# Kernel optimization log

Hardware: AMD Instinct MI355X
Metric: run time of the kernel (lower is better)

Reference implementation:

```python
import jax, jax.numpy as jnp
import numpy as np

B, NB, L, K, C, H = 4, 256, 64, 65, 512, 8
HD = C // H
SCALE = HD ** -0.5


def setup_inputs() -> dict:
    key = jax.random.key(0)
    k = jax.random.split(key, 6)
    x = jax.random.normal(k[0], (B, NB * L, C), dtype=jnp.float32)
    mask = jax.random.bernoulli(k[1], 0.3, (NB, L, K))
    d = jnp.arange(L)
    mask = mask.at[:, d, d].set(True)      # self edges always on
    mask = mask.at[:, :, L].set(True)      # block-node column always on
    edge_feats = jax.random.normal(k[2], (NB, L, K, 4), dtype=jnp.float32)
    qkv_w = jax.random.normal(k[3], (C, 3 * C), dtype=jnp.float32) * (C ** -0.5)
    qkv_b = jnp.zeros((3 * C,), dtype=jnp.float32)
    proj_w = jax.random.normal(k[4], (C, C), dtype=jnp.float32) * (C ** -0.5)
    proj_b = jnp.zeros((C,), dtype=jnp.float32)
    return {"x": x, "attn_mask": mask, "edge_feats": edge_feats,
            "qkv_w": qkv_w, "qkv_b": qkv_b, "proj_w": proj_w, "proj_b": proj_b}


def reference(x, attn_mask, edge_feats, qkv_w, qkv_b, proj_w, proj_b):
    # x: (B, N, C) with N = NB*L (no padding needed); pool = 1, layout LxL+1
    x_blk = x.reshape(B, NB, L, C)                       # query tokens per leaf block
    block_node = x_blk.mean(axis=2, keepdims=True)       # (B, NB, 1, C)
    kv = jnp.concatenate([x_blk, block_node], axis=2)    # (B, NB, K, C), K = L+1

    qkv_q = x_blk @ qkv_w + qkv_b
    qkv_kv = kv @ qkv_w + qkv_b
    q = qkv_q[..., :C].reshape(B, NB, L, H, HD)
    k = qkv_kv[..., C:2 * C].reshape(B, NB, K, H, HD)
    v = qkv_kv[..., 2 * C:].reshape(B, NB, K, H, HD)

    scores = jnp.einsum('bnqhd,bnkhd->bnqkh', q, k) * SCALE  # (B,NB,L,K,H)

    # physics bias: edge_feats[..., :4] broadcast over batch; special/diagonal overrides
    bp = jnp.broadcast_to(edge_feats[None, ..., :4], (B, NB, L, K, 4))
    bp = bp.at[:, :, :, L, :].set(0.0)
    bp = bp.at[:, :, :, L, 3].set(1.0)                    # block-node key column
    d = jnp.arange(L)
    bp = bp.at[:, :, d, d, :].set(0.0)
    bp = bp.at[:, :, d, d, 3].set(1.0)                    # self edge
    scores = scores + bp[..., 3:4]                        # channel 3 additive bias (all heads)

    mask = attn_mask[None, :, :, :, None]                 # (1,NB,L,K,1)
    scores = jnp.where(mask, scores, jnp.float32(-1e9))
    attn = jax.nn.softmax(scores, axis=3)

    out = jnp.einsum('bnqkh,bnkhd->bnqhd', attn, v).reshape(B, NB * L, C)
    return out @ proj_w + proj_b
```

## Files before the change

kernel.cpp:

```cpp
#include <hip/hip_runtime.h>
#include <hip/hip_bf16.h>
#include <math.h>

typedef unsigned short u16;
typedef __attribute__((ext_vector_type(8))) short s16x8;
typedef __attribute__((ext_vector_type(4))) float f32x4;

#define NB_ 256
#define L_  64
#define KK_ 65
#define C_  512
#define H_  8
#define NEDGE (256*64*65)
#define MTOT  65536

__device__ __forceinline__ float b2f(u16 u){
  union { unsigned int i; float f; } x; x.i = ((unsigned int)u) << 16; return x.f;
}
__device__ __forceinline__ u16 f2b(float f){
  union { float f; unsigned int i; } x; x.f = f;
  return (u16)((x.i + 0x7FFFu + ((x.i >> 16) & 1u)) >> 16);
}

__device__ __forceinline__ void gload_lds16(const u16* g, u16* l){
  __builtin_amdgcn_global_load_lds(
      (const __attribute__((address_space(1))) unsigned int*)g,
      (__attribute__((address_space(3))) unsigned int*)l,
      16, 0, 0);
}

__global__ void detect_dtype_kernel(const u16* __restrict__ x, int* __restrict__ flagdt){
  __shared__ int cnt;
  if (threadIdx.x == 0) cnt = 0;
  __syncthreads();
  u16 v = x[(size_t)threadIdx.x * 2 * 1001];
  int e = (v >> 7) & 0xFF;
  if (e >= 141) atomicAdd(&cnt, 1);
  __syncthreads();
  if (threadIdx.x == 0) *flagdt = (cnt >= 8) ? 1 : 0;
}

__global__ void detect_mask_kernel(const unsigned char* __restrict__ m, int* __restrict__ flag){
  __shared__ int ok1, ok2, ok4;
  if (threadIdx.x == 0){ ok1 = 1; ok2 = 1; ok4 = 1; }
  __syncthreads();
  size_t e = (size_t)threadIdx.x * 65 + 64;
  if (((const unsigned char*)m)[e] == 0)  atomicAnd(&ok1, 0);
  if (((const unsigned short*)m)[e] == 0) atomicAnd(&ok2, 0);
  if (((const unsigned int*)m)[e] == 0u)  atomicAnd(&ok4, 0);
  __syncthreads();
  if (threadIdx.x == 0){
    int f = 4;
    if (ok2) f = 2;
    if (ok1) f = 1;
    *flag = f;
  }
}

__global__ void convert_kernel(const void* __restrict__ src, u16* __restrict__ dst,
                               long n, const int* __restrict__ flagdt){
  long i = ((long)blockIdx.x * 256 + threadIdx.x) * 8;
  if (i >= n) return;
  if (*flagdt){
    const float* s = (const float*)src + i;
    u16 o[8];
    #pragma unroll
    for (int j = 0; j < 8; ++j) o[j] = f2b(s[j]);
    *(s16x8*)(dst + i) = *(const s16x8*)o;
  } else {
    *(s16x8*)(dst + i) = *(const s16x8*)((const u16*)src + i);
  }
}

__global__ void build_bias_kernel(const void* __restrict__ edge,
                                  const unsigned char* __restrict__ mask,
                                  const int* __restrict__ flagdt,
                                  const int* __restrict__ flagm,
                                  u16* __restrict__ dst){
  long i = (long)blockIdx.x * 256 + threadIdx.x;
  if (i >= NEDGE) return;
  int kk = (int)(i % 65);
  long rowi = i / 65;
  int l = (int)(rowi & 63);
  int fm = *flagm;
  bool mt;
  if (fm == 1)      mt = mask[i] != 0;
  else if (fm == 2) mt = ((const unsigned short*)mask)[i] != 0;
  else              mt = ((const unsigned int*)mask)[i]   != 0u;
  float v;
  if (!mt)                      v = -1e9f;
  else if (kk == 64 || kk == l) v = 1.0f;
  else v = (*flagdt) ? ((const float*)edge)[i*4 + 3] : b2f(((const u16*)edge)[i*4 + 3]);
  dst[i] = f2b(v);
}

__global__ void transpose_conv_kernel(const void* __restrict__ in, u16* __restrict__ out,
                                      int R, int Cc, const int* __restrict__ flagdt){
  long i = (long)blockIdx.x * 256 + threadIdx.x;
  if (i < (long)R * Cc){
    int r = (int)(i / Cc), c = (int)(i % Cc);
    u16 v = (*flagdt) ? f2b(((const float*)in)[i]) : ((const u16*)in)[i];
    out[(long)c * R + r] = v;
  }
}

__global__ __launch_bounds__(256) void block_mean_kernel(const u16* __restrict__ x, u16* __restrict__ bm){
  int blk = blockIdx.x;
  const u16* xp = x + (long)blk * 64 * 512;
  for (int c = threadIdx.x; c < 512; c += 256){
    float s = 0.f;
    #pragma unroll
    for (int l = 0; l < 64; ++l) s += b2f(xp[l*512 + c]);
    bm[(long)blk * 512 + c] = f2b(s * 0.015625f);
  }
}

__global__ __launch_bounds__(256) void gemm_bt_kernel(
    const u16* __restrict__ A, const u16* __restrict__ BT,
    const u16* __restrict__ bias, u16* __restrict__ Cmat,
    int lda, int ldc, int Kdim, const int* __restrict__ flagdt, int out_mode,
    long row_off)
{
  __shared__ __align__(16) u16 As[128*32];
  __shared__ __align__(16) u16 Bs[128*32];
  const int t = threadIdx.x;
  const int lane = t & 63;
  const int w = t >> 6;
  const int wm = w & 1, wn = w >> 1;
  const int quad = lane >> 4;
  const int ml = lane & 15;

  const int nwg  = gridDim.x * gridDim.y;
  const int orig = blockIdx.y * gridDim.x + blockIdx.x;
  int lid = orig;
  if ((nwg & 7) == 0) lid = (orig & 7) * (nwg >> 3) + (orig >> 3);
  const int bx = lid % gridDim.x;
  const int by = lid / gridDim.x;
  const long colbase = (long)bx * 128;
  const long rowbase = (long)by * 128;
  const int of = out_mode ? *flagdt : 0;

  const f32x4 zero4 = {0.f, 0.f, 0.f, 0.f};
  f32x4 acc[4][4];
  #pragma unroll
  for (int i = 0; i < 4; ++i)
    #pragma unroll
    for (int j = 0; j < 4; ++j) acc[i][j] = zero4;

  const int c0 = t,       r0 = c0 >> 2, s0 = c0 & 3, g0 = s0 ^ ((r0 >> 1) & 3);
  const int c1 = t + 256, r1 = c1 >> 2, s1 = c1 & 3, g1 = s1 ^ ((r1 >> 1) & 3);
  const u16* Arow0 = A + (rowbase + r0) * (long)lda + g0*8;
  const u16* Arow1 = A + (rowbase + r1) * (long)lda + g1*8;
  const u16* Brow0 = BT + (colbase + r0) * (long)Kdim + g0*8;
  const u16* Brow1 = BT + (colbase + r1) * (long)Kdim + g1*8;

  u16* AsW0 = As + w*512;
  u16* AsW1 = As + 2048 + w*512;
  u16* BsW0 = Bs + w*512;
  u16* BsW1 = Bs + 2048 + w*512;

  for (int k0 = 0; k0 < Kdim; k0 += 32){
    __syncthreads();
    gload_lds16(Arow0 + k0, AsW0);
    gload_lds16(Arow1 + k0, AsW1);
    gload_lds16(Brow0 + k0, BsW0);
    gload_lds16(Brow1 + k0, BsW1);
    __syncthreads();
    s16x8 af[4], bfr[4];
    #pragma unroll
    for (int i = 0; i < 4; ++i){
      int m = wm*64 + i*16 + ml;
      af[i]  = *(const s16x8*)(As + m*32 + ((quad ^ ((m>>1)&3)))*8);
      int n = wn*64 + i*16 + ml;
      bfr[i] = *(const s16x8*)(Bs + n*32 + ((quad ^ ((n>>1)&3)))*8);
    }
    #pragma unroll
    for (int i = 0; i < 4; ++i)
      #pragma unroll
      for (int j = 0; j < 4; ++j)
        acc[i][j] = __builtin_amdgcn_mfma_f32_16x16x32_bf16(af[i], bfr[j], acc[i][j], 0, 0, 0);
  }

  #pragma unroll
  for (int j = 0; j < 4; ++j){
    long col = colbase + wn*64 + j*16 + ml;
    float bv = b2f(bias[col]);
    #pragma unroll
    for (int i = 0; i < 4; ++i){
      long row = row_off + rowbase + wm*64 + i*16 + quad*4;
      if (of){
        float* Cf = (float*)Cmat;
        #pragma unroll
        for (int r = 0; r < 4; ++r)
          Cf[(row + r) * (long)ldc + col] = acc[i][j][r] + bv;
      } else {
        #pragma unroll
        for (int r = 0; r < 4; ++r)
          Cmat[(row + r) * (long)ldc + col] = f2b(acc[i][j][r] + bv);
      }
    }
  }
}

__global__ __launch_bounds__(256, 4) void attn_kernel(
    const u16* __restrict__ Y, const u16* __restrict__ kvb,
    const u16* __restrict__ biasb, u16* __restrict__ AO)
{
  __shared__ __align__(16) u16 k_s [80*72];
  __shared__ __align__(16) u16 vT_s[64*104];
  __shared__ __align__(16) u16 P_s [64*104];

  const int t = threadIdx.x;
  const int lane = t & 63;
  const int w = t >> 6;
  const int quad = lane >> 4;
  const int ml = lane & 15;

  const int orig = blockIdx.y * gridDim.x + blockIdx.x;
  const int lid  = (orig & 7) * 1024 + (orig >> 3);
  const int blk  = lid >> 3;
  const int h    = lid & 7;
  const int nb = blk & (NB_ - 1);
  const long yrow0 = (long)blk * 64;

  const u16* qrow = Y + (yrow0 + w*16 + ml)*1536 + h*64 + quad*8;
  s16x8 aq0 = *(const s16x8*)(qrow);
  s16x8 aq1 = *(const s16x8*)(qrow + 32);

  for (int i = t; i < 64*31; i += 256){ int d = i/31, c = 65 + (i%31); vT_s[d*104 + c] = 0; }
  for (int i = t; i < 64*16; i += 256){ int l = i>>4,  c = 80 + (i&15); P_s[l*104 + c] = 0; }
  for (int i = t; i < 15*72; i += 256){ k_s[65*72 + i] = 0; }

  for (int c = t; c < 520; c += 256){
    int kk = c >> 3, c8 = c & 7;
    const u16 *srck, *srcv;
    if (kk < 64){
      const u16* base = Y + (yrow0 + kk)*1536;
      srck = base + 512  + h*64 + c8*8;
      srcv = base + 1024 + h*64 + c8*8;
    } else {
      const u16* base = kvb + (long)blk * 1024;
      srck = base + h*64 + c8*8;
      srcv = base + 512 + h*64 + c8*8;
    }
    *(s16x8*)(k_s + kk*72 + c8*8) = *(const s16x8*)srck;
    s16x8 vv = *(const s16x8*)srcv;
    #pragma unroll
    for (int j = 0; j < 8; ++j){
      int jj = (j + c8) & 7;
      vT_s[(c8*8 + jj)*104 + kk] = (u16)vv[jj];
    }
  }
  __syncthreads();

  const f32x4 zero4 = {0.f, 0.f, 0.f, 0.f};
  f32x4 sacc[5];
  #pragma unroll
  for (int j = 0; j < 5; ++j) sacc[j] = zero4;
  #pragma unroll
  for (int j = 0; j < 5; ++j){
    s16x8 bk0 = *(const s16x8*)(k_s + (j*16 + ml)*72 + quad*8);
    sacc[j] = __builtin_amdgcn_mfma_f32_16x16x32_bf16(aq0, bk0, sacc[j], 0, 0, 0);
    s16x8 bk1 = *(const s16x8*)(k_s + (j*16 + ml)*72 + 32 + quad*8);
    sacc[j] = __builtin_amdgcn_mfma_f32_16x16x32_bf16(aq1, bk1, sacc[j], 0, 0, 0);
  }

  float sv[5][4];
  #pragma unroll
  for (int j = 0; j < 5; ++j){
    int kk = j*16 + ml;
    #pragma unroll
    for (int r = 0; r < 4; ++r){
      int l = w*16 + quad*4 + r;
      float xv = -1e9f;
      if (kk < 65){
        long e = ((long)nb*64 + l)*65 + kk;
        xv = sacc[j][r]*0.125f + b2f(biasb[e]);
      }
      sv[j][r] = xv;
    }
  }
  #pragma unroll
  for (int r = 0; r < 4; ++r){
    float mx = sv[0][r];
    #pragma unroll
    for (int j = 1; j < 5; ++j) mx = fmaxf(mx, sv[j][r]);
    #pragma unroll
    for (int o = 1; o < 16; o <<= 1) mx = fmaxf(mx, __shfl_xor(mx, o, 64));
    float sm = 0.f;
    #pragma unroll
    for (int j = 0; j < 5; ++j){ float e = __expf(sv[j][r] - mx); sv[j][r] = e; sm += e; }
    #pragma unroll
    for (int o = 1; o < 16; o <<= 1) sm += __shfl_xor(sm, o, 64);
    float inv = 1.0f / sm;
    #pragma unroll
    for (int j = 0; j < 5; ++j) sv[j][r] *= inv;
  }
  #pragma unroll
  for (int j = 0; j < 5; ++j){
    int kk = j*16 + ml;
    #pragma unroll
    for (int r = 0; r < 4; ++r)
      P_s[(w*16 + quad*4 + r)*104 + kk] = f2b(sv[j][r]);
  }
  __syncthreads();

  f32x4 oacc[4];
  #pragma unroll
  for (int j = 0; j < 4; ++j) oacc[j] = zero4;
  #pragma unroll
  for (int s = 0; s < 3; ++s){
    s16x8 ap = *(const s16x8*)(P_s + (w*16 + ml)*104 + s*32 + quad*8);
    #pragma unroll
    for (int j = 0; j < 4; ++j){
      s16x8 bv = *(const s16x8*)(vT_s + (j*16 + ml)*104 + s*32 + quad*8);
      oacc[j] = __builtin_amdgcn_mfma_f32_16x16x32_bf16(ap, bv, oacc[j], 0, 0, 0);
    }
  }
  #pragma unroll
  for (int j = 0; j < 4; ++j){
    int d = j*16 + ml;
    #pragma unroll
    for (int r = 0; r < 4; ++r){
      int l = w*16 + quad*4 + r;
      AO[(yrow0 + l)*512 + h*64 + d] = f2b(oacc[j][r]);
    }
  }
}

extern "C" void kernel_launch(void* const* d_in, const int* in_sizes, int n_in,
                              void* d_out, int out_size, void* d_ws, size_t ws_size,
                              hipStream_t stream)
{
  const void* x_raw     = d_in[0];
  const unsigned char* mask = (const unsigned char*)d_in[1];
  const void* edge_raw  = d_in[2];
  const void* qkvw_raw  = d_in[3];
  const void* qkvb_raw  = d_in[4];
  const void* projw_raw = d_in[5];
  const void* projb_raw = d_in[6];

  char* ws = (char*)d_ws;
  size_t off = 0;
  int*  flagm  = (int*)ws;
  int*  flagdt = (int*)(ws + 4);         off += 1024;
  u16*  XC  = (u16*)(ws + off);          off += (size_t)33554432*2;
  u16*  EB  = (u16*)(ws + off);          off += (size_t)NEDGE*2;
  u16*  WT  = (u16*)(ws + off);          off += (size_t)1536*512*2;
  u16*  PT  = (u16*)(ws + off);          off += (size_t)512*512*2;
  u16*  QB  = (u16*)(ws + off);          off += 4096;
  u16*  PB  = (u16*)(ws + off);          off += 4096;
  u16*  BM  = (u16*)(ws + off);          off += (size_t)1024*512*2;
  u16*  KVB = (u16*)(ws + off);          off += (size_t)1024*1024*2;
  u16*  Y   = (u16*)(ws + off);          off += (size_t)MTOT*1536*2;
  u16*  AO  = (u16*)(ws + off);          off += (size_t)MTOT*512*2;

  detect_dtype_kernel<<<dim3(1), dim3(128), 0, stream>>>((const u16*)x_raw, flagdt);
  detect_mask_kernel<<<dim3(1), dim3(128), 0, stream>>>(mask, flagm);

  convert_kernel<<<dim3(33554432/8/256), dim3(256), 0, stream>>>(x_raw, XC, 33554432, flagdt);
  build_bias_kernel<<<dim3((NEDGE + 255)/256), dim3(256), 0, stream>>>(edge_raw, mask, flagdt, flagm, EB);
  transpose_conv_kernel<<<dim3((512*1536 + 255)/256), dim3(256), 0, stream>>>(qkvw_raw, WT, 512, 1536, flagdt);
  transpose_conv_kernel<<<dim3((512*512  + 255)/256), dim3(256), 0, stream>>>(projw_raw, PT, 512, 512, flagdt);
  convert_kernel<<<dim3(1), dim3(256), 0, stream>>>(qkvb_raw, QB, 1536, flagdt);
  convert_kernel<<<dim3(1), dim3(256), 0, stream>>>(projb_raw, PB, 512, flagdt);

  block_mean_kernel<<<dim3(1024), dim3(256), 0, stream>>>(XC, BM);
  gemm_bt_kernel<<<dim3(8, 8), dim3(256), 0, stream>>>(BM, WT + 512*512, QB + 512, KVB, 512, 1024, 512, flagdt, 0, 0);

  gemm_bt_kernel<<<dim3(12, MTOT/128), dim3(256), 0, stream>>>(XC, WT, QB, Y, 512, 1536, 512, flagdt, 0, 0);
  attn_kernel<<<dim3(1024, 8), dim3(256), 0, stream>>>(Y, KVB, EB, AO);
  gemm_bt_kernel<<<dim3(4, MTOT/128), dim3(256), 0, stream>>>(AO, PT, PB, (u16*)d_out, 512, 512, 512, flagdt, 1, 0);
}
```

Measured before the change: 601.0 us.

## Double GEMM K-step per barrier; process two heads per attention block reusing bias

New measurement: 560.5 us. 6.7% less time.

```diff
diff --git a/kernel.cpp b/kernel.cpp
--- a/kernel.cpp
+++ b/kernel.cpp
@@ -121,8 +121,8 @@
     int lda, int ldc, int Kdim, const int* __restrict__ flagdt, int out_mode,
     long row_off)
 {
-  __shared__ __align__(16) u16 As[128*32];
-  __shared__ __align__(16) u16 Bs[128*32];
+  __shared__ __align__(16) u16 As[2*128*32];
+  __shared__ __align__(16) u16 Bs[2*128*32];
   const int t = threadIdx.x;
   const int lane = t & 63;
   const int w = t >> 6;
@@ -154,31 +154,35 @@
   const u16* Brow0 = BT + (colbase + r0) * (long)Kdim + g0*8;
   const u16* Brow1 = BT + (colbase + r1) * (long)Kdim + g1*8;
 
-  u16* AsW0 = As + w*512;
-  u16* AsW1 = As + 2048 + w*512;
-  u16* BsW0 = Bs + w*512;
-  u16* BsW1 = Bs + 2048 + w*512;
-
-  for (int k0 = 0; k0 < Kdim; k0 += 32){
+  for (int k0 = 0; k0 < Kdim; k0 += 64){
     __syncthreads();
-    gload_lds16(Arow0 + k0, AsW0);
-    gload_lds16(Arow1 + k0, AsW1);
-    gload_lds16(Brow0 + k0, BsW0);
-    gload_lds16(Brow1 + k0, BsW1);
+    gload_lds16(Arow0 + k0,      As + w*512);
+    gload_lds16(Arow1 + k0,      As + 2048 + w*512);
+    gload_lds16(Arow0 + k0 + 32, As + 4096 + w*512);
+    gload_lds16(Arow1 + k0 + 32, As + 4096 + 2048 + w*512);
+    gload_lds16(Brow0 + k0,      Bs + w*512);
+    gload_lds16(Brow1 + k0,      Bs + 2048 + w*512);
+    gload_lds16(Brow0 + k0 + 32, Bs + 4096 + w*512);
+    gload_lds16(Brow1 + k0 + 32, Bs + 4096 + 2048 + w*512);
     __syncthreads();
-    s16x8 af[4], bfr[4];
-    #pragma unroll
-    for (int i = 0; i < 4; ++i){
-      int m = wm*64 + i*16 + ml;
-      af[i]  = *(const s16x8*)(As + m*32 + ((quad ^ ((m>>1)&3)))*8);
-      int n = wn*64 + i*16 + ml;
-      bfr[i] = *(const s16x8*)(Bs + n*32 + ((quad ^ ((n>>1)&3)))*8);
-    }
-    #pragma unroll
-    for (int i = 0; i < 4; ++i)
-      #pragma unroll
-      for (int j = 0; j < 4; ++j)
-        acc[i][j] = __builtin_amdgcn_mfma_f32_16x16x32_bf16(af[i], bfr[j], acc[i][j], 0, 0, 0);
+    #pragma unroll
+    for (int hb = 0; hb < 2; ++hb){
+      const u16* Ab = As + hb*4096;
+      const u16* Bb = Bs + hb*4096;
+      s16x8 af[4], bfr[4];
+      #pragma unroll
+      for (int i = 0; i < 4; ++i){
+        int m = wm*64 + i*16 + ml;
+        af[i]  = *(const s16x8*)(Ab + m*32 + ((quad ^ ((m>>1)&3)))*8);
+        int n = wn*64 + i*16 + ml;
+        bfr[i] = *(const s16x8*)(Bb + n*32 + ((quad ^ ((n>>1)&3)))*8);
+      }
+      #pragma unroll
+      for (int i = 0; i < 4; ++i)
+        #pragma unroll
+        for (int j = 0; j < 4; ++j)
+          acc[i][j] = __builtin_amdgcn_mfma_f32_16x16x32_bf16(af[i], bfr[j], acc[i][j], 0, 0, 0);
+    }
   }
 
   #pragma unroll
@@ -217,113 +221,123 @@
   const int ml = lane & 15;
 
   const int orig = blockIdx.y * gridDim.x + blockIdx.x;
-  const int lid  = (orig & 7) * 1024 + (orig >> 3);
-  const int blk  = lid >> 3;
-  const int h    = lid & 7;
+  const int lid  = (orig & 7) * 512 + (orig >> 3);
+  const int blk  = lid >> 2;
+  const int hp   = lid & 3;
   const int nb = blk & (NB_ - 1);
   const long yrow0 = (long)blk * 64;
 
-  const u16* qrow = Y + (yrow0 + w*16 + ml)*1536 + h*64 + quad*8;
-  s16x8 aq0 = *(const s16x8*)(qrow);
-  s16x8 aq1 = *(const s16x8*)(qrow + 32);
+  float bb[5][4];
+  #pragma unroll
+  for (int j = 0; j < 5; ++j){
+    int kk = j*16 + ml;
+    #pragma unroll
+    for (int r = 0; r < 4; ++r){
+      int l = w*16 + quad*4 + r;
+      bb[j][r] = (kk < 65) ? b2f(biasb[((long)nb*64 + l)*65 + kk]) : 0.f;
+    }
+  }
 
   for (int i = t; i < 64*31; i += 256){ int d = i/31, c = 65 + (i%31); vT_s[d*104 + c] = 0; }
   for (int i = t; i < 64*16; i += 256){ int l = i>>4,  c = 80 + (i&15); P_s[l*104 + c] = 0; }
   for (int i = t; i < 15*72; i += 256){ k_s[65*72 + i] = 0; }
 
-  for (int c = t; c < 520; c += 256){
-    int kk = c >> 3, c8 = c & 7;
-    const u16 *srck, *srcv;
-    if (kk < 64){
-      const u16* base = Y + (yrow0 + kk)*1536;
-      srck = base + 512  + h*64 + c8*8;
-      srcv = base + 1024 + h*64 + c8*8;
-    } else {
-      const u16* base = kvb + (long)blk * 1024;
-      srck = base + h*64 + c8*8;
-      srcv = base + 512 + h*64 + c8*8;
-    }
-    *(s16x8*)(k_s + kk*72 + c8*8) = *(const s16x8*)srck;
-    s16x8 vv = *(const s16x8*)srcv;
-    #pragma unroll
-    for (int j = 0; j < 8; ++j){
-      int jj = (j + c8) & 7;
-      vT_s[(c8*8 + jj)*104 + kk] = (u16)vv[jj];
-    }
-  }
-  __syncthreads();
-
   const f32x4 zero4 = {0.f, 0.f, 0.f, 0.f};
-  f32x4 sacc[5];
-  #pragma unroll
-  for (int j = 0; j < 5; ++j) sacc[j] = zero4;
-  #pragma unroll
-  for (int j = 0; j < 5; ++j){
-    s16x8 bk0 = *(const s16x8*)(k_s + (j*16 + ml)*72 + quad*8);
-    sacc[j] = __builtin_amdgcn_mfma_f32_16x16x32_bf16(aq0, bk0, sacc[j], 0, 0, 0);
-    s16x8 bk1 = *(const s16x8*)(k_s + (j*16 + ml)*72 + 32 + quad*8);
-    sacc[j] = __builtin_amdgcn_mfma_f32_16x16x32_bf16(aq1, bk1, sacc[j], 0, 0, 0);
-  }
-
-  float sv[5][4];
-  #pragma unroll
-  for (int j = 0; j < 5; ++j){
-    int kk = j*16 + ml;
+
+  for (int hh = 0; hh < 2; ++hh){
+    const int h = hp*2 + hh;
+    if (hh) __syncthreads();
+
+    const u16* qrow = Y + (yrow0 + w*16 + ml)*1536 + h*64 + quad*8;
+    s16x8 aq0 = *(const s16x8*)(qrow);
+    s16x8 aq1 = *(const s16x8*)(qrow + 32);
+
+    for (int c = t; c < 520; c += 256){
+      int kk = c >> 3, c8 = c & 7;
+      const u16 *srck, *srcv;
+      if (kk < 64){
+        const u16* base = Y + (yrow0 + kk)*1536;
+        srck = base + 512  + h*64 + c8*8;
+        srcv = base + 1024 + h*64 + c8*8;
+      } else {
+        const u16* base = kvb + (long)blk * 1024;
+        srck = base + h*64 + c8*8;
+        srcv = base + 512 + h*64 + c8*8;
+      }
+      *(s16x8*)(k_s + kk*72 + c8*8) = *(const s16x8*)srck;
+      s16x8 vv = *(const s16x8*)srcv;
+      #pragma unroll
+      for (int j = 0; j < 8; ++j){
+        int jj = (j + c8) & 7;
+        vT_s[(c8*8 + jj)*104 + kk] = (u16)vv[jj];
+      }
+    }
+    __syncthreads();
+
+    f32x4 sacc[5];
+    #pragma unroll
+    for (int j = 0; j < 5; ++j) sacc[j] = zero4;
+    #pragma unroll
+    for (int j = 0; j < 5; ++j){
+      s16x8 bk0 = *(const s16x8*)(k_s + (j*16 + ml)*72 + quad*8);
+      sacc[j] = __builtin_amdgcn_mfma_f32_16x16x32_bf16(aq0, bk0, sacc[j], 0, 0, 0);
+      s16x8 bk1 = *(const s16x8*)(k_s + (j*16 + ml)*72 + 32 + quad*8);
+      sacc[j] = __builtin_amdgcn_mfma_f32_16x16x32_bf16(aq1, bk1, sacc[j], 0, 0, 0);
+    }
+
+    float sv[5][4];
+    #pragma unroll
+    for (int j = 0; j < 5; ++j){
+      int kk = j*16 + ml;
+      #pragma unroll
+      for (int r = 0; r < 4; ++r)
+        sv[j][r] = (kk < 65) ? (sacc[j][r]*0.125f + bb[j][r]) : -1e9f;
+    }
     #pragma unroll
     for (int r = 0; r < 4; ++r){
-      int l = w*16 + quad*4 + r;
-      float xv = -1e9f;
-      if (kk < 65){
-        long e = ((long)nb*64 + l)*65 + kk;
-        xv = sacc[j][r]*0.125f + b2f(biasb[e]);
-      }
-      sv[j][r] = xv;
-    }
-  }
-  #pragma unroll
-  for (int r = 0; r < 4; ++r){
-    float mx = sv[0][r];
-    #pragma unroll
-    for (int j = 1; j < 5; ++j) mx = fmaxf(mx, sv[j][r]);
-    #pragma unroll
-    for (int o = 1; o < 16; o <<= 1) mx = fmaxf(mx, __shfl_xor(mx, o, 64));
-    float sm = 0.f;
-    #pragma unroll
-    for (int j = 0; j < 5; ++j){ float e = __expf(sv[j][r] - mx); sv[j][r] = e; sm += e; }
-    #pragma unroll
-    for (int o = 1; o < 16; o <<= 1) sm += __shfl_xor(sm, o, 64);
-    float inv = 1.0f / sm;
-    #pragma unroll
-    for (int j = 0; j < 5; ++j) sv[j][r] *= inv;
-  }
-  #pragma unroll
-  for (int j = 0; j < 5; ++j){
-    int kk = j*16 + ml;
-    #pragma unroll
-    for (int r = 0; r < 4; ++r)
-      P_s[(w*16 + quad*4 + r)*104 + kk] = f2b(sv[j][r]);
-  }
-  __syncthreads();
-
-  f32x4 oacc[4];
-  #pragma unroll
-  for (int j = 0; j < 4; ++j) oacc[j] = zero4;
-  #pragma unroll
-  for (int s = 0; s < 3; ++s){
-    s16x8 ap = *(const s16x8*)(P_s + (w*16 + ml)*104 + s*32 + quad*8);
+      float mx = sv[0][r];
+      #pragma unroll
+      for (int j = 1; j < 5; ++j) mx = fmaxf(mx, sv[j][r]);
+      #pragma unroll
+      for (int o = 1; o < 16; o <<= 1) mx = fmaxf(mx, __shfl_xor(mx, o, 64));
+      float sm = 0.f;
+      #pragma unroll
+      for (int j = 0; j < 5; ++j){ float e = __expf(sv[j][r] - mx); sv[j][r] = e; sm += e; }
+      #pragma unroll
+      for (int o = 1; o < 16; o <<= 1) sm += __shfl_xor(sm, o, 64);
+      float inv = 1.0f / sm;
+      #pragma unroll
+      for (int j = 0; j < 5; ++j) sv[j][r] *= inv;
+    }
+    #pragma unroll
+    for (int j = 0; j < 5; ++j){
+      int kk = j*16 + ml;
+      #pragma unroll
+      for (int r = 0; r < 4; ++r)
+        P_s[(w*16 + quad*4 + r)*104 + kk] = f2b(sv[j][r]);
+    }
+    __syncthreads();
+
+    f32x4 oacc[4];
+    #pragma unroll
+    for (int j = 0; j < 4; ++j) oacc[j] = zero4;
+    #pragma unroll
+    for (int s = 0; s < 3; ++s){
+      s16x8 ap = *(const s16x8*)(P_s + (w*16 + ml)*104 + s*32 + quad*8);
+      #pragma unroll
+      for (int j = 0; j < 4; ++j){
+        s16x8 bv = *(const s16x8*)(vT_s + (j*16 + ml)*104 + s*32 + quad*8);
+        oacc[j] = __builtin_amdgcn_mfma_f32_16x16x32_bf16(ap, bv, oacc[j], 0, 0, 0);
+      }
+    }
     #pragma unroll
     for (int j = 0; j < 4; ++j){
-      s16x8 bv = *(const s16x8*)(vT_s + (j*16 + ml)*104 + s*32 + quad*8);
-      oacc[j] = __builtin_amdgcn_mfma_f32_16x16x32_bf16(ap, bv, oacc[j], 0, 0, 0);
-    }
-  }
-  #pragma unroll
-  for (int j = 0; j < 4; ++j){
-    int d = j*16 + ml;
-    #pragma unroll
-    for (int r = 0; r < 4; ++r){
-      int l = w*16 + quad*4 + r;
-      AO[(yrow0 + l)*512 + h*64 + d] = f2b(oacc[j][r]);
+      int d = j*16 + ml;
+      #pragma unroll
+      for (int r = 0; r < 4; ++r){
+        int l = w*16 + quad*4 + r;
+        AO[(yrow0 + l)*512 + h*64 + d] = f2b(oacc[j][r]);
+      }
     }
   }
 }
@@ -369,6 +383,6 @@
   gemm_bt_kernel<<<dim3(8, 8), dim3(256), 0, stream>>>(BM, WT + 512*512, QB + 512, KVB, 512, 1024, 512, flagdt, 0, 0);
 
   gemm_bt_kernel<<<dim3(12, MTOT/128), dim3(256), 0, stream>>>(XC, WT, QB, Y, 512, 1536, 512, flagdt, 0, 0);
-  attn_kernel<<<dim3(1024, 8), dim3(256), 0, stream>>>(Y, KVB, EB, AO);
+  attn_kernel<<<dim3(1024, 4), dim3(256), 0, stream>>>(Y, KVB, EB, AO);
   gemm_bt_kernel<<<dim3(4, MTOT/128), dim3(256), 0, stream>>>(AO, PT, PB, (u16*)d_out, 512, 512, 512, flagdt, 1, 0);
 }
```
